# Kernel optimization log

Measured on AMD Instinct MI355X. Metric: run time of the kernel, lower is better.

## Reference

```python
import jax, jax.numpy as jnp
import numpy as np

DIM = 64  # per-head dim used for the sqrt scale


def setup_inputs() -> dict:
    key = jax.random.key(0)
    kq, kk, kv, ke, kf = jax.random.split(key, 5)
    B, N, d, k = 32, 4096, 64, 256
    Q = jax.random.normal(kq, (B, N, d), dtype=jnp.float32)
    K = jax.random.normal(kk, (B, N, d), dtype=jnp.float32)
    V = jax.random.normal(kv, (B, N, d), dtype=jnp.float32)
    E = jax.random.normal(ke, (N, k), dtype=jnp.float32) * (1.0 / np.sqrt(N))
    F = jax.random.normal(kf, (N, k), dtype=jnp.float32) * (1.0 / np.sqrt(N))
    return {"Q": Q, "K": K, "V": V, "E": E, "F": F}


def reference(Q, K, V, E, F):
    # Linformer head: K^T E -> [B,d,k]; Q (K^T E) / sqrt(d) -> [B,N,k]
    K_proj = jnp.einsum('bnd,nk->bdk', K, E)          # low-rank key projection
    scores = jnp.einsum('bnd,bdk->bnk', Q, K_proj) / jnp.sqrt(jnp.float32(DIM))
    P_bar = jax.nn.softmax(scores, axis=2)            # [B,N,k]
    # (V^T F)^T -> [B,k,d]
    V_proj = jnp.einsum('bnd,nk->bkd', V, F)
    return jnp.einsum('bnk,bkd->bnd', P_bar, V_proj)  # [B,N,d]
```

## Files before the change

### kernel.cpp

```cpp
#include <hip/hip_runtime.h>
#include <hip/hip_bf16.h>

#define BB 32
#define NN 4096
#define DDIM 64
#define KKR 256

typedef __attribute__((ext_vector_type(8)))  short bf16x8;
typedef __attribute__((ext_vector_type(16))) float f32x16;
typedef __attribute__((ext_vector_type(4)))  float f32x4;

static __device__ inline unsigned short f2bf(float x) {
  union { float f; unsigned u; } v; v.f = x;
  unsigned r = (v.u + 0x7FFFu + ((v.u >> 16) & 1u)) >> 16;
  return (unsigned short)r;
}

static __device__ inline unsigned packbf2(float a, float b) {
  union { float f; unsigned u; } x, y; x.f = a; y.f = b;
  unsigned ua = x.u + 0x7FFFu + ((x.u >> 16) & 1u);
  unsigned ub = y.u + 0x7FFFu + ((y.u >> 16) & 1u);
  return (ua >> 16) | (ub & 0xFFFF0000u);
}

__global__ __launch_bounds__(256) void pass0_kernel(
    const float* __restrict__ K, const float* __restrict__ V,
    const float* __restrict__ E, const float* __restrict__ F,
    unsigned short* __restrict__ KT, unsigned short* __restrict__ VT,
    unsigned short* __restrict__ ET, unsigned short* __restrict__ FT)
{
  const int id = blockIdx.x;
  const int t  = threadIdx.x;
  const float* src; unsigned short* dst; int stride, n0, col0;
  if (id < 2048) {
    int b = id >> 6, nt = id & 63;
    src = K + (long)b * NN * DDIM; dst = KT + (long)b * DDIM * NN;
    stride = 64; n0 = nt * 64; col0 = 0;
  } else if (id < 4096) {
    int i2 = id - 2048; int b = i2 >> 6, nt = i2 & 63;
    src = V + (long)b * NN * DDIM; dst = VT + (long)b * DDIM * NN;
    stride = 64; n0 = nt * 64; col0 = 0;
  } else if (id < 4352) {
    int i2 = id - 4096; int nt = i2 >> 2, ct = i2 & 3;
    src = E; dst = ET; stride = 256; n0 = nt * 64; col0 = ct * 64;
  } else {
    int i2 = id - 4352; int nt = i2 >> 2, ct = i2 & 3;
    src = F; dst = FT; stride = 256; n0 = nt * 64; col0 = ct * 64;
  }
  const int c = t & 63;
  const int q = t >> 6;
  const float* sp = src + (long)(n0 + q * 16) * stride + col0 + c;
  float v[16];
#pragma unroll
  for (int j = 0; j < 16; ++j) v[j] = sp[(long)j * stride];
  unsigned short o[16];
#pragma unroll
  for (int j = 0; j < 16; ++j) o[j] = f2bf(v[j]);
  unsigned short* dp = dst + (long)(col0 + c) * NN + n0 + q * 16;
  *(bf16x8*)dp       = *(const bf16x8*)&o[0];
  *(bf16x8*)(dp + 8) = *(const bf16x8*)&o[8];
}

__global__ __launch_bounds__(256, 2) void proj_gemm(
    const unsigned short* __restrict__ KT, const unsigned short* __restrict__ VT,
    const unsigned short* __restrict__ ET, const unsigned short* __restrict__ FT,
    float* __restrict__ KpP, float* __restrict__ VpP)
{
  extern __shared__ unsigned short sm[];
  const int blk = blockIdx.x;
  const int chunk = blk & 3, mat = (blk >> 2) & 1, b = blk >> 3;
  const int t = threadIdx.x, w = t >> 6, l = t & 63, h = l >> 5, lr = l & 31;

  const unsigned short *Ag, *Bg; int M; float* Cg;
  if (mat == 0) {
    Ag = ET; Bg = KT + (long)b * DDIM * NN; M = 256;
    Cg = KpP + (long)chunk * (BB * 16384) + b * 16384;
  } else {
    Ag = VT + (long)b * DDIM * NN; Bg = FT; M = 64;
    Cg = VpP + (long)chunk * (BB * 16384) + b * 16384;
  }
  const int mt0 = (mat == 0) ? 2 * w : 0;
  const int nt0 = (mat == 0) ? 0 : 2 * w;

  f32x16 acc[2][2];
#pragma unroll
  for (int i = 0; i < 2; ++i)
#pragma unroll
    for (int j = 0; j < 2; ++j)
#pragma unroll
      for (int q = 0; q < 16; ++q) acc[i][j][q] = 0.f;

  const int n0 = chunk * 1024;
  for (int stg = 0; stg < 16; ++stg) {
    const int nb = n0 + stg * 64;
    __syncthreads();
#pragma unroll
    for (int i = 0; i < 10; ++i) {
      int cidx = i * 256 + t;
      int row = cidx >> 3, off = cidx & 7;
      const unsigned short* g =
          (row < M ? Ag + (long)row * NN : Bg + (long)(row - M) * NN) + nb + off * 8;
      *(bf16x8*)&sm[row * 72 + off * 8] = *(const bf16x8*)g;
    }
    __syncthreads();
#pragma unroll
    for (int kk = 0; kk < 4; ++kk) {
      bf16x8 a0 = *(const bf16x8*)&sm[(mt0 * 32 + lr) * 72 + kk * 16 + h * 8];
      bf16x8 a1 = *(const bf16x8*)&sm[((mt0 + 1) * 32 + lr) * 72 + kk * 16 + h * 8];
      bf16x8 b0 = *(const bf16x8*)&sm[(M + nt0 * 32 + lr) * 72 + kk * 16 + h * 8];
      bf16x8 b1 = *(const bf16x8*)&sm[(M + (nt0 + 1) * 32 + lr) * 72 + kk * 16 + h * 8];
      acc[0][0] = __builtin_amdgcn_mfma_f32_32x32x16_bf16(a0, b0, acc[0][0], 0, 0, 0);
      acc[0][1] = __builtin_amdgcn_mfma_f32_32x32x16_bf16(a0, b1, acc[0][1], 0, 0, 0);
      acc[1][0] = __builtin_amdgcn_mfma_f32_32x32x16_bf16(a1, b0, acc[1][0], 0, 0, 0);
      acc[1][1] = __builtin_amdgcn_mfma_f32_32x32x16_bf16(a1, b1, acc[1][1], 0, 0, 0);
    }
  }
#pragma unroll
  for (int mt = 0; mt < 2; ++mt)
#pragma unroll
    for (int nt = 0; nt < 2; ++nt)
#pragma unroll
      for (int i = 0; i < 16; ++i) {
        int row = (mt0 + mt) * 32 + (i & 3) + 8 * (i >> 2) + 4 * h;
        int col = (nt0 + nt) * 32 + lr;
        int idx = (mat == 0) ? row * 64 + col : row * 256 + col;
        Cg[idx] = acc[mt][nt][i];
      }
}

__global__ __launch_bounds__(256) void reduce_cvt(
    const float* __restrict__ KpP, const float* __restrict__ VpP,
    unsigned short* __restrict__ Kpb, unsigned short* __restrict__ Vpb)
{
  const int blk = blockIdx.x;
  const float* src = (blk < 256) ? KpP : VpP;
  unsigned short* dst = (blk < 256) ? Kpb : Vpb;
  const long i = (long)(blk & 255) * 2048 + threadIdx.x * 8;
  float a[8];
#pragma unroll
  for (int j = 0; j < 8; ++j) a[j] = 0.f;
#pragma unroll
  for (int cch = 0; cch < 4; ++cch) {
    const float4 p0 = *(const float4*)(src + (long)cch * (BB * 16384) + i);
    const float4 p1 = *(const float4*)(src + (long)cch * (BB * 16384) + i + 4);
    a[0] += p0.x; a[1] += p0.y; a[2] += p0.z; a[3] += p0.w;
    a[4] += p1.x; a[5] += p1.y; a[6] += p1.z; a[7] += p1.w;
  }
  unsigned short o[8];
#pragma unroll
  for (int j = 0; j < 8; ++j) o[j] = f2bf(a[j]);
  *(bf16x8*)(dst + i) = *(const bf16x8*)&o[0];
}

__global__ __launch_bounds__(256, 2) void attn2_kernel(
    const float* __restrict__ Qg, const unsigned short* __restrict__ Kpb,
    const unsigned short* __restrict__ Vpb, float* __restrict__ Og)
{
  __shared__ float O_lds[128 * 64];

  const int blk = blockIdx.x;
  const int b = blk >> 5, rg = blk & 31;
  const int t = threadIdx.x, w = t >> 6, l = t & 63;
  const int h = l >> 5, lr = l & 31;
  const int rbase = rg * 128 + w * 32;

  const float* Qrow = Qg + ((long)b * NN + rbase + lr) * 64;
  bf16x8 Bq[4];
#pragma unroll
  for (int kk = 0; kk < 4; ++kk) {
    float4 x = *(const float4*)(Qrow + kk * 16 + h * 8);
    float4 y = *(const float4*)(Qrow + kk * 16 + h * 8 + 4);
    unsigned short u[8];
    u[0] = f2bf(x.x); u[1] = f2bf(x.y); u[2] = f2bf(x.z); u[3] = f2bf(x.w);
    u[4] = f2bf(y.x); u[5] = f2bf(y.y); u[6] = f2bf(y.z); u[7] = f2bf(y.w);
    Bq[kk] = *(const bf16x8*)u;
  }

  const unsigned short* Kp = Kpb + (long)b * 16384;
  const unsigned short* Vp = Vpb + (long)b * 16384;

  union UV { uint4 u; bf16x8 v; };
  bf16x8 Bp[16];
  float rowpart = 0.f;

#pragma unroll
  for (int kt = 0; kt < 8; ++kt) {
    f32x16 s;
#pragma unroll
    for (int q = 0; q < 16; ++q) s[q] = 0.f;
#pragma unroll
    for (int kk = 0; kk < 4; ++kk) {
      bf16x8 A = *(const bf16x8*)(Kp + (long)(kt * 32 + lr) * 64 + kk * 16 + h * 8);
      s = __builtin_amdgcn_mfma_f32_32x32x16_bf16(A, Bq[kk], s, 0, 0, 0);
    }
    float p[16];
#pragma unroll
    for (int q = 0; q < 16; ++q) {
      p[q] = exp2f(s[q] * 0.1803368801f);
      rowpart += p[q];
    }
    unsigned wv[8];
#pragma unroll
    for (int m = 0; m < 8; ++m) wv[m] = packbf2(p[2 * m], p[2 * m + 1]);
    unsigned r02 = __shfl_xor(h ? wv[0] : wv[2], 32);
    unsigned r13 = __shfl_xor(h ? wv[1] : wv[3], 32);
    unsigned r46 = __shfl_xor(h ? wv[4] : wv[6], 32);
    unsigned r57 = __shfl_xor(h ? wv[5] : wv[7], 32);
    UV c0, c1;
    if (h == 0) {
      c0.u = uint4{wv[0], wv[1], r02, r13};
      c1.u = uint4{wv[4], wv[5], r46, r57};
    } else {
      c0.u = uint4{r02, r13, wv[2], wv[3]};
      c1.u = uint4{r46, r57, wv[6], wv[7]};
    }
    Bp[kt * 2 + 0] = c0.v;
    Bp[kt * 2 + 1] = c1.v;
  }
  float rowsum = rowpart + __shfl_xor(rowpart, 32);

  f32x16 o[2];
#pragma unroll
  for (int mt = 0; mt < 2; ++mt)
#pragma unroll
    for (int q = 0; q < 16; ++q) o[mt][q] = 0.f;
#pragma unroll
  for (int kc = 0; kc < 16; ++kc) {
    bf16x8 A0 = *(const bf16x8*)(Vp + (long)lr * 256 + kc * 16 + h * 8);
    bf16x8 A1 = *(const bf16x8*)(Vp + (long)(32 + lr) * 256 + kc * 16 + h * 8);
    o[0] = __builtin_amdgcn_mfma_f32_32x32x16_bf16(A0, Bp[kc], o[0], 0, 0, 0);
    o[1] = __builtin_amdgcn_mfma_f32_32x32x16_bf16(A1, Bp[kc], o[1], 0, 0, 0);
  }

  const float inv = __builtin_amdgcn_rcpf(rowsum);
  const int r = w * 32 + lr;
#pragma unroll
  for (int mt = 0; mt < 2; ++mt)
#pragma unroll
    for (int qg = 0; qg < 4; ++qg) {
      f32x4 vq;
      vq[0] = o[mt][qg * 4 + 0] * inv;
      vq[1] = o[mt][qg * 4 + 1] * inv;
      vq[2] = o[mt][qg * 4 + 2] * inv;
      vq[3] = o[mt][qg * 4 + 3] * inv;
      int cd = 8 * mt + 2 * qg + h;
      int cp = cd ^ (r & 15);
      *(f32x4*)&O_lds[r * 64 + cp * 4] = vq;
    }
  __syncthreads();

  const long obase = ((long)b * NN + rg * 128) * 64;
#pragma unroll
  for (int i = 0; i < 8; ++i) {
    int ci = i * 256 + t;
    int rr = ci >> 4, cc = ci & 15, cp = cc ^ (rr & 15);
    *(float4*)(Og + obase + rr * 64 + cc * 4) = *(const float4*)&O_lds[rr * 64 + cp * 4];
  }
}

extern "C" void kernel_launch(void* const* d_in, const int* in_sizes, int n_in,
                              void* d_out, int out_size, void* d_ws, size_t ws_size,
                              hipStream_t stream) {
  const float* Q = (const float*)d_in[0];
  const float* K = (const float*)d_in[1];
  const float* V = (const float*)d_in[2];
  const float* E = (const float*)d_in[3];
  const float* F = (const float*)d_in[4];
  float* out = (float*)d_out;

  char* ws = (char*)d_ws;
  float*          KpP = (float*)(ws);
  float*          VpP = (float*)(ws + (8l << 20));
  unsigned short* Kpb = (unsigned short*)(ws + (16l << 20));
  unsigned short* Vpb = (unsigned short*)(ws + (17l << 20));
  unsigned short* KT  = (unsigned short*)(ws + (18l << 20));
  unsigned short* VT  = (unsigned short*)(ws + (34l << 20));
  unsigned short* ET  = (unsigned short*)(ws + (50l << 20));
  unsigned short* FT  = (unsigned short*)(ws + (52l << 20));

  pass0_kernel<<<dim3(4608), dim3(256), 0, stream>>>(K, V, E, F, KT, VT, ET, FT);

  hipFuncSetAttribute((const void*)proj_gemm,
                      hipFuncAttributeMaxDynamicSharedMemorySize, 46080);
  proj_gemm<<<dim3(256), dim3(256), 46080, stream>>>(KT, VT, ET, FT, KpP, VpP);

  reduce_cvt<<<dim3(512), dim3(256), 0, stream>>>(KpP, VpP, Kpb, Vpb);

  attn2_kernel<<<dim3(1024), dim3(256), 0, stream>>>(Q, Kpb, Vpb, out);
}
```

Measured before the change: 221.8 us.

## Drop transpose pass, load fp32 directly in projection GEMM, fuse attention loops

Removes the separate transpose-and-convert pass. The projection GEMM now reads fp32 K/V/E/F straight from global memory with strided per-lane loads, converts them to bf16 in registers and skips LDS staging, so the extra round trip through workspace is gone. The attention kernel handles 256 rows per block with two row tiles per wave. It fuses the score, exp and PV MFMAs per key tile instead of buffering all probabilities, and reuses the K/V projection fragments across both row tiles. The risks are uncoalesced strided global loads in the GEMM, higher register pressure, and 64KB of LDS per attention block, which may limit occupancy.

After: 202.1 us. 8.9% less time.

```diff
diff --git a/kernel.cpp b/kernel.cpp
--- a/kernel.cpp
+++ b/kernel.cpp
@@ -4,7 +4,6 @@
 #define BB 32
 #define NN 4096
 #define DDIM 64
-#define KKR 256
 
 typedef __attribute__((ext_vector_type(8)))  short bf16x8;
 typedef __attribute__((ext_vector_type(16))) float f32x16;
@@ -16,116 +15,85 @@
   return (unsigned short)r;
 }
 
-static __device__ inline unsigned packbf2(float a, float b) {
-  union { float f; unsigned u; } x, y; x.f = a; y.f = b;
-  unsigned ua = x.u + 0x7FFFu + ((x.u >> 16) & 1u);
-  unsigned ub = y.u + 0x7FFFu + ((y.u >> 16) & 1u);
-  return (ua >> 16) | (ub & 0xFFFF0000u);
-}
-
-__global__ __launch_bounds__(256) void pass0_kernel(
-    const float* __restrict__ K, const float* __restrict__ V,
-    const float* __restrict__ E, const float* __restrict__ F,
-    unsigned short* __restrict__ KT, unsigned short* __restrict__ VT,
-    unsigned short* __restrict__ ET, unsigned short* __restrict__ FT)
-{
-  const int id = blockIdx.x;
-  const int t  = threadIdx.x;
-  const float* src; unsigned short* dst; int stride, n0, col0;
-  if (id < 2048) {
-    int b = id >> 6, nt = id & 63;
-    src = K + (long)b * NN * DDIM; dst = KT + (long)b * DDIM * NN;
-    stride = 64; n0 = nt * 64; col0 = 0;
-  } else if (id < 4096) {
-    int i2 = id - 2048; int b = i2 >> 6, nt = i2 & 63;
-    src = V + (long)b * NN * DDIM; dst = VT + (long)b * DDIM * NN;
-    stride = 64; n0 = nt * 64; col0 = 0;
-  } else if (id < 4352) {
-    int i2 = id - 4096; int nt = i2 >> 2, ct = i2 & 3;
-    src = E; dst = ET; stride = 256; n0 = nt * 64; col0 = ct * 64;
-  } else {
-    int i2 = id - 4352; int nt = i2 >> 2, ct = i2 & 3;
-    src = F; dst = FT; stride = 256; n0 = nt * 64; col0 = ct * 64;
-  }
-  const int c = t & 63;
-  const int q = t >> 6;
-  const float* sp = src + (long)(n0 + q * 16) * stride + col0 + c;
-  float v[16];
-#pragma unroll
-  for (int j = 0; j < 16; ++j) v[j] = sp[(long)j * stride];
-  unsigned short o[16];
-#pragma unroll
-  for (int j = 0; j < 16; ++j) o[j] = f2bf(v[j]);
-  unsigned short* dp = dst + (long)(col0 + c) * NN + n0 + q * 16;
-  *(bf16x8*)dp       = *(const bf16x8*)&o[0];
-  *(bf16x8*)(dp + 8) = *(const bf16x8*)&o[8];
-}
-
-__global__ __launch_bounds__(256, 2) void proj_gemm(
-    const unsigned short* __restrict__ KT, const unsigned short* __restrict__ VT,
-    const unsigned short* __restrict__ ET, const unsigned short* __restrict__ FT,
+static __device__ inline unsigned pk(float a, float b) {
+  union { __hip_bfloat162 h; unsigned u; } c;
+  c.h = __float22bfloat162_rn(float2{a, b});
+  return c.u;
+}
+
+static __device__ inline bf16x8 pack8(const float* f) {
+  union { unsigned u[4]; bf16x8 v; } r;
+  r.u[0] = pk(f[0], f[1]); r.u[1] = pk(f[2], f[3]);
+  r.u[2] = pk(f[4], f[5]); r.u[3] = pk(f[6], f[7]);
+  return r.v;
+}
+
+template <int SA, int SB, int OS>
+static __device__ inline void proj_body(
+    const float* __restrict__ As, const float* __restrict__ Bs,
+    float* __restrict__ Cg, int mAdd, int nAdd, int chunk, int h, int lr)
+{
+  f32x16 acc[2][2];
+#pragma unroll
+  for (int i = 0; i < 2; ++i)
+#pragma unroll
+    for (int j = 0; j < 2; ++j)
+#pragma unroll
+      for (int q = 0; q < 16; ++q) acc[i][j][q] = 0.f;
+
+  const int n0 = chunk * 1024 + h * 8;
+  const float* pA = As + (long)n0 * SA + mAdd + lr;
+  const float* pB = Bs + (long)n0 * SB + nAdd + lr;
+
+#pragma unroll 2
+  for (int tt = 0; tt < 64; ++tt) {
+    const float* qA = pA + (long)tt * 16 * SA;
+    const float* qB = pB + (long)tt * 16 * SB;
+    float a0[8], a1[8], b0[8], b1[8];
+#pragma unroll
+    for (int j = 0; j < 8; ++j) {
+      a0[j] = qA[j * SA];      a1[j] = qA[j * SA + 32];
+      b0[j] = qB[j * SB];      b1[j] = qB[j * SB + 32];
+    }
+    bf16x8 A0 = pack8(a0), A1 = pack8(a1);
+    bf16x8 B0 = pack8(b0), B1 = pack8(b1);
+    acc[0][0] = __builtin_amdgcn_mfma_f32_32x32x16_bf16(A0, B0, acc[0][0], 0, 0, 0);
+    acc[0][1] = __builtin_amdgcn_mfma_f32_32x32x16_bf16(A0, B1, acc[0][1], 0, 0, 0);
+    acc[1][0] = __builtin_amdgcn_mfma_f32_32x32x16_bf16(A1, B0, acc[1][0], 0, 0, 0);
+    acc[1][1] = __builtin_amdgcn_mfma_f32_32x32x16_bf16(A1, B1, acc[1][1], 0, 0, 0);
+  }
+
+#pragma unroll
+  for (int mt = 0; mt < 2; ++mt)
+#pragma unroll
+    for (int nt = 0; nt < 2; ++nt)
+#pragma unroll
+      for (int i = 0; i < 16; ++i) {
+        int ro  = (i & 3) + 8 * (i >> 2) + 4 * h;
+        int row = mAdd + mt * 32 + ro;
+        int col = nAdd + nt * 32 + lr;
+        Cg[row * OS + col] = acc[mt][nt][i];
+      }
+}
+
+__global__ __launch_bounds__(256) void proj_gemm(
+    const float* __restrict__ Kg, const float* __restrict__ Vg,
+    const float* __restrict__ Eg, const float* __restrict__ Fg,
     float* __restrict__ KpP, float* __restrict__ VpP)
 {
-  extern __shared__ unsigned short sm[];
   const int blk = blockIdx.x;
   const int chunk = blk & 3, mat = (blk >> 2) & 1, b = blk >> 3;
   const int t = threadIdx.x, w = t >> 6, l = t & 63, h = l >> 5, lr = l & 31;
 
-  const unsigned short *Ag, *Bg; int M; float* Cg;
   if (mat == 0) {
-    Ag = ET; Bg = KT + (long)b * DDIM * NN; M = 256;
-    Cg = KpP + (long)chunk * (BB * 16384) + b * 16384;
+    proj_body<256, 64, 64>(Eg, Kg + (long)b * NN * DDIM,
+                           KpP + (long)chunk * (BB * 16384) + b * 16384,
+                           w * 64, 0, chunk, h, lr);
   } else {
-    Ag = VT + (long)b * DDIM * NN; Bg = FT; M = 64;
-    Cg = VpP + (long)chunk * (BB * 16384) + b * 16384;
-  }
-  const int mt0 = (mat == 0) ? 2 * w : 0;
-  const int nt0 = (mat == 0) ? 0 : 2 * w;
-
-  f32x16 acc[2][2];
-#pragma unroll
-  for (int i = 0; i < 2; ++i)
-#pragma unroll
-    for (int j = 0; j < 2; ++j)
-#pragma unroll
-      for (int q = 0; q < 16; ++q) acc[i][j][q] = 0.f;
-
-  const int n0 = chunk * 1024;
-  for (int stg = 0; stg < 16; ++stg) {
-    const int nb = n0 + stg * 64;
-    __syncthreads();
-#pragma unroll
-    for (int i = 0; i < 10; ++i) {
-      int cidx = i * 256 + t;
-      int row = cidx >> 3, off = cidx & 7;
-      const unsigned short* g =
-          (row < M ? Ag + (long)row * NN : Bg + (long)(row - M) * NN) + nb + off * 8;
-      *(bf16x8*)&sm[row * 72 + off * 8] = *(const bf16x8*)g;
-    }
-    __syncthreads();
-#pragma unroll
-    for (int kk = 0; kk < 4; ++kk) {
-      bf16x8 a0 = *(const bf16x8*)&sm[(mt0 * 32 + lr) * 72 + kk * 16 + h * 8];
-      bf16x8 a1 = *(const bf16x8*)&sm[((mt0 + 1) * 32 + lr) * 72 + kk * 16 + h * 8];
-      bf16x8 b0 = *(const bf16x8*)&sm[(M + nt0 * 32 + lr) * 72 + kk * 16 + h * 8];
-      bf16x8 b1 = *(const bf16x8*)&sm[(M + (nt0 + 1) * 32 + lr) * 72 + kk * 16 + h * 8];
-      acc[0][0] = __builtin_amdgcn_mfma_f32_32x32x16_bf16(a0, b0, acc[0][0], 0, 0, 0);
-      acc[0][1] = __builtin_amdgcn_mfma_f32_32x32x16_bf16(a0, b1, acc[0][1], 0, 0, 0);
-      acc[1][0] = __builtin_amdgcn_mfma_f32_32x32x16_bf16(a1, b0, acc[1][0], 0, 0, 0);
-      acc[1][1] = __builtin_amdgcn_mfma_f32_32x32x16_bf16(a1, b1, acc[1][1], 0, 0, 0);
-    }
-  }
-#pragma unroll
-  for (int mt = 0; mt < 2; ++mt)
-#pragma unroll
-    for (int nt = 0; nt < 2; ++nt)
-#pragma unroll
-      for (int i = 0; i < 16; ++i) {
-        int row = (mt0 + mt) * 32 + (i & 3) + 8 * (i >> 2) + 4 * h;
-        int col = (nt0 + nt) * 32 + lr;
-        int idx = (mat == 0) ? row * 64 + col : row * 256 + col;
-        Cg[idx] = acc[mt][nt][i];
-      }
+    proj_body<64, 256, 256>(Vg + (long)b * NN * DDIM, Fg,
+                            VpP + (long)chunk * (BB * 16384) + b * 16384,
+                            0, w * 64, chunk, h, lr);
+  }
 }
 
 __global__ __launch_bounds__(256) void reduce_cvt(
@@ -156,102 +124,116 @@
     const float* __restrict__ Qg, const unsigned short* __restrict__ Kpb,
     const unsigned short* __restrict__ Vpb, float* __restrict__ Og)
 {
-  __shared__ float O_lds[128 * 64];
+  extern __shared__ float O_lds[];
 
   const int blk = blockIdx.x;
-  const int b = blk >> 5, rg = blk & 31;
+  const int b = blk >> 4, rg = blk & 15;
   const int t = threadIdx.x, w = t >> 6, l = t & 63;
   const int h = l >> 5, lr = l & 31;
-  const int rbase = rg * 128 + w * 32;
-
-  const float* Qrow = Qg + ((long)b * NN + rbase + lr) * 64;
-  bf16x8 Bq[4];
-#pragma unroll
-  for (int kk = 0; kk < 4; ++kk) {
-    float4 x = *(const float4*)(Qrow + kk * 16 + h * 8);
-    float4 y = *(const float4*)(Qrow + kk * 16 + h * 8 + 4);
-    unsigned short u[8];
-    u[0] = f2bf(x.x); u[1] = f2bf(x.y); u[2] = f2bf(x.z); u[3] = f2bf(x.w);
-    u[4] = f2bf(y.x); u[5] = f2bf(y.y); u[6] = f2bf(y.z); u[7] = f2bf(y.w);
-    Bq[kk] = *(const bf16x8*)u;
-  }
+  const int rbase = rg * 256 + w * 64;
 
   const unsigned short* Kp = Kpb + (long)b * 16384;
   const unsigned short* Vp = Vpb + (long)b * 16384;
 
+  bf16x8 Bq[2][4];
+#pragma unroll
+  for (int rt = 0; rt < 2; ++rt)
+#pragma unroll
+    for (int kk = 0; kk < 4; ++kk) {
+      const float* qp = Qg + ((long)b * NN + rbase + rt * 32 + lr) * 64 + kk * 16 + h * 8;
+      float4 x = *(const float4*)qp;
+      float4 y = *(const float4*)(qp + 4);
+      union { unsigned u[4]; bf16x8 v; } r;
+      r.u[0] = pk(x.x, x.y); r.u[1] = pk(x.z, x.w);
+      r.u[2] = pk(y.x, y.y); r.u[3] = pk(y.z, y.w);
+      Bq[rt][kk] = r.v;
+    }
+
+  f32x16 o[2][2];
+#pragma unroll
+  for (int rt = 0; rt < 2; ++rt)
+#pragma unroll
+    for (int dt = 0; dt < 2; ++dt)
+#pragma unroll
+      for (int q = 0; q < 16; ++q) o[rt][dt][q] = 0.f;
+  float rowpart[2] = {0.f, 0.f};
+
   union UV { uint4 u; bf16x8 v; };
-  bf16x8 Bp[16];
-  float rowpart = 0.f;
 
 #pragma unroll
   for (int kt = 0; kt < 8; ++kt) {
-    f32x16 s;
-#pragma unroll
-    for (int q = 0; q < 16; ++q) s[q] = 0.f;
-#pragma unroll
-    for (int kk = 0; kk < 4; ++kk) {
-      bf16x8 A = *(const bf16x8*)(Kp + (long)(kt * 32 + lr) * 64 + kk * 16 + h * 8);
-      s = __builtin_amdgcn_mfma_f32_32x32x16_bf16(A, Bq[kk], s, 0, 0, 0);
+    bf16x8 Ak[4];
+#pragma unroll
+    for (int kk = 0; kk < 4; ++kk)
+      Ak[kk] = *(const bf16x8*)(Kp + (long)(kt * 32 + lr) * 64 + kk * 16 + h * 8);
+    bf16x8 Av[2][2];
+#pragma unroll
+    for (int dt = 0; dt < 2; ++dt)
+#pragma unroll
+      for (int kc = 0; kc < 2; ++kc)
+        Av[dt][kc] = *(const bf16x8*)(Vp + (long)(dt * 32 + lr) * 256 + (kt * 2 + kc) * 16 + h * 8);
+
+#pragma unroll
+    for (int rt = 0; rt < 2; ++rt) {
+      f32x16 s;
+#pragma unroll
+      for (int q = 0; q < 16; ++q) s[q] = 0.f;
+#pragma unroll
+      for (int kk = 0; kk < 4; ++kk)
+        s = __builtin_amdgcn_mfma_f32_32x32x16_bf16(Ak[kk], Bq[rt][kk], s, 0, 0, 0);
+
+      float p[16];
+#pragma unroll
+      for (int q = 0; q < 16; ++q) p[q] = exp2f(s[q] * 0.1803368801f);
+      rowpart[rt] += (((p[0] + p[1]) + (p[2] + p[3])) + ((p[4] + p[5]) + (p[6] + p[7])))
+                   + (((p[8] + p[9]) + (p[10] + p[11])) + ((p[12] + p[13]) + (p[14] + p[15])));
+
+      unsigned wv[8];
+#pragma unroll
+      for (int m = 0; m < 8; ++m) wv[m] = pk(p[2 * m], p[2 * m + 1]);
+      unsigned r02 = __shfl_xor(h ? wv[0] : wv[2], 32);
+      unsigned r13 = __shfl_xor(h ? wv[1] : wv[3], 32);
+      unsigned r46 = __shfl_xor(h ? wv[4] : wv[6], 32);
+      unsigned r57 = __shfl_xor(h ? wv[5] : wv[7], 32);
+      UV c0, c1;
+      if (h == 0) {
+        c0.u = uint4{wv[0], wv[1], r02, r13};
+        c1.u = uint4{wv[4], wv[5], r46, r57};
+      } else {
+        c0.u = uint4{r02, r13, wv[2], wv[3]};
+        c1.u = uint4{r46, r57, wv[6], wv[7]};
+      }
+      o[rt][0] = __builtin_amdgcn_mfma_f32_32x32x16_bf16(Av[0][0], c0.v, o[rt][0], 0, 0, 0);
+      o[rt][0] = __builtin_amdgcn_mfma_f32_32x32x16_bf16(Av[0][1], c1.v, o[rt][0], 0, 0, 0);
+      o[rt][1] = __builtin_amdgcn_mfma_f32_32x32x16_bf16(Av[1][0], c0.v, o[rt][1], 0, 0, 0);
+      o[rt][1] = __builtin_amdgcn_mfma_f32_32x32x16_bf16(Av[1][1], c1.v, o[rt][1], 0, 0, 0);
     }
-    float p[16];
-#pragma unroll
-    for (int q = 0; q < 16; ++q) {
-      p[q] = exp2f(s[q] * 0.1803368801f);
-      rowpart += p[q];
-    }
-    unsigned wv[8];
-#pragma unroll
-    for (int m = 0; m < 8; ++m) wv[m] = packbf2(p[2 * m], p[2 * m + 1]);
-    unsigned r02 = __shfl_xor(h ? wv[0] : wv[2], 32);
-    unsigned r13 = __shfl_xor(h ? wv[1] : wv[3], 32);
-    unsigned r46 = __shfl_xor(h ? wv[4] : wv[6], 32);
-    unsigned r57 = __shfl_xor(h ? wv[5] : wv[7], 32);
-    UV c0, c1;
-    if (h == 0) {
-      c0.u = uint4{wv[0], wv[1], r02, r13};
-      c1.u = uint4{wv[4], wv[5], r46, r57};
-    } else {
-      c0.u = uint4{r02, r13, wv[2], wv[3]};
-      c1.u = uint4{r46, r57, wv[6], wv[7]};
-    }
-    Bp[kt * 2 + 0] = c0.v;
-    Bp[kt * 2 + 1] = c1.v;
-  }
-  float rowsum = rowpart + __shfl_xor(rowpart, 32);
-
-  f32x16 o[2];
-#pragma unroll
-  for (int mt = 0; mt < 2; ++mt)
-#pragma unroll
-    for (int q = 0; q < 16; ++q) o[mt][q] = 0.f;
-#pragma unroll
-  for (int kc = 0; kc < 16; ++kc) {
-    bf16x8 A0 = *(const bf16x8*)(Vp + (long)lr * 256 + kc * 16 + h * 8);
-    bf16x8 A1 = *(const bf16x8*)(Vp + (long)(32 + lr) * 256 + kc * 16 + h * 8);
-    o[0] = __builtin_amdgcn_mfma_f32_32x32x16_bf16(A0, Bp[kc], o[0], 0, 0, 0);
-    o[1] = __builtin_amdgcn_mfma_f32_32x32x16_bf16(A1, Bp[kc], o[1], 0, 0, 0);
-  }
-
-  const float inv = __builtin_amdgcn_rcpf(rowsum);
-  const int r = w * 32 + lr;
-#pragma unroll
-  for (int mt = 0; mt < 2; ++mt)
-#pragma unroll
-    for (int qg = 0; qg < 4; ++qg) {
-      f32x4 vq;
-      vq[0] = o[mt][qg * 4 + 0] * inv;
-      vq[1] = o[mt][qg * 4 + 1] * inv;
-      vq[2] = o[mt][qg * 4 + 2] * inv;
-      vq[3] = o[mt][qg * 4 + 3] * inv;
-      int cd = 8 * mt + 2 * qg + h;
-      int cp = cd ^ (r & 15);
-      *(f32x4*)&O_lds[r * 64 + cp * 4] = vq;
-    }
+  }
+
+#pragma unroll
+  for (int rt = 0; rt < 2; ++rt) {
+    float rowsum = rowpart[rt] + __shfl_xor(rowpart[rt], 32);
+    float inv = __builtin_amdgcn_rcpf(rowsum);
+    const int r = w * 64 + rt * 32 + lr;
+#pragma unroll
+    for (int dt = 0; dt < 2; ++dt)
+#pragma unroll
+      for (int qg = 0; qg < 4; ++qg) {
+        f32x4 vq;
+        vq[0] = o[rt][dt][qg * 4 + 0] * inv;
+        vq[1] = o[rt][dt][qg * 4 + 1] * inv;
+        vq[2] = o[rt][dt][qg * 4 + 2] * inv;
+        vq[3] = o[rt][dt][qg * 4 + 3] * inv;
+        int cd = dt * 8 + 2 * qg + h;
+        int cp = cd ^ (r & 15);
+        *(f32x4*)&O_lds[r * 64 + cp * 4] = vq;
+      }
+  }
   __syncthreads();
 
-  const long obase = ((long)b * NN + rg * 128) * 64;
-#pragma unroll
-  for (int i = 0; i < 8; ++i) {
+  const long obase = ((long)b * NN + rg * 256) * 64;
+#pragma unroll
+  for (int i = 0; i < 16; ++i) {
     int ci = i * 256 + t;
     int rr = ci >> 4, cc = ci & 15, cp = cc ^ (rr & 15);
     *(float4*)(Og + obase + rr * 64 + cc * 4) = *(const float4*)&O_lds[rr * 64 + cp * 4];
@@ -273,18 +255,12 @@
   float*          VpP = (float*)(ws + (8l << 20));
   unsigned short* Kpb = (unsigned short*)(ws + (16l << 20));
   unsigned short* Vpb = (unsigned short*)(ws + (17l << 20));
-  unsigned short* KT  = (unsigned short*)(ws + (18l << 20));
-  unsigned short* VT  = (unsigned short*)(ws + (34l << 20));
-  unsigned short* ET  = (unsigned short*)(ws + (50l << 20));
-  unsigned short* FT  = (unsigned short*)(ws + (52l << 20));
-
-  pass0_kernel<<<dim3(4608), dim3(256), 0, stream>>>(K, V, E, F, KT, VT, ET, FT);
-
-  hipFuncSetAttribute((const void*)proj_gemm,
-                      hipFuncAttributeMaxDynamicSharedMemorySize, 46080);
-  proj_gemm<<<dim3(256), dim3(256), 46080, stream>>>(KT, VT, ET, FT, KpP, VpP);
+
+  proj_gemm<<<dim3(256), dim3(256), 0, stream>>>(K, V, E, F, KpP, VpP);
 
   reduce_cvt<<<dim3(512), dim3(256), 0, stream>>>(KpP, VpP, Kpb, Vpb);
 
-  attn2_kernel<<<dim3(1024), dim3(256), 0, stream>>>(Q, Kpb, Vpb, out);
-}
+  hipFuncSetAttribute((const void*)attn2_kernel,
+                      hipFuncAttributeMaxDynamicSharedMemorySize, 65536);
+  attn2_kernel<<<dim3(512), dim3(256), 65536, stream>>>(Q, Kpb, Vpb, out);
+}
```
